# Optimization experiments

Measured on AMD Instinct MI355X. Metric: run time of the kernel, lower is better.

The kernel has to match this reference:

```python
import jax, jax.numpy as jnp
import numpy as np


def setup_inputs() -> dict:
    key = jax.random.key(0)
    k = jax.random.split(key, 5)
    B, L, D = 8, 2048, 256  # D = 2*d_model, c_len == q_len == L (required by source's s1 broadcast)
    c = jax.random.normal(k[0], (B, L, D), dtype=jnp.float32)
    q = jax.random.normal(k[1], (B, L, D), dtype=jnp.float32)
    c_weight = jax.random.normal(k[2], (D, 1), dtype=jnp.float32) * 0.05
    q_weight = jax.random.normal(k[3], (D, 1), dtype=jnp.float32) * 0.05
    cq_weight = jax.random.normal(k[4], (1, 1, D), dtype=jnp.float32) * 0.05
    bias = jnp.zeros((1,), dtype=jnp.float32)
    return {"c": c, "q": q, "c_weight": c_weight, "q_weight": q_weight,
            "cq_weight": cq_weight, "bias": bias}


def reference(c, q, c_weight, q_weight, cq_weight, bias):
    # Dropout omitted (identity) for a deterministic reference.
    # s0: [B, c_len, 1] -> broadcasts over q_len
    s0 = jnp.matmul(c, c_weight)                       # [B, L, 1]
    # s1 (faithful to source, which uses c here): [B, 1, c_len]
    s1 = jnp.swapaxes(jnp.matmul(c, q_weight), 1, 2)   # [B, 1, L]
    # s2: elementwise-scaled batched GEMM: [B, c_len, q_len]
    s2 = jnp.matmul(c * cq_weight, jnp.swapaxes(q, 1, 2))
    s = s0 + s1 + s2 + bias                            # broadcast sum + scalar bias
    return s
```

## Files before the change

### kernel.cpp

```cpp
#include <hip/hip_runtime.h>
#include <hip/hip_bf16.h>

#define B_ 8
#define L_ 2048
#define D_ 256

typedef __bf16 bf16x8 __attribute__((ext_vector_type(8)));
typedef float f32x4 __attribute__((ext_vector_type(4)));

static __device__ __forceinline__ unsigned short f2bf(float f) {
    unsigned int u = __builtin_bit_cast(unsigned int, f);
    unsigned int lsb = (u >> 16) & 1u;
    u += 0x7fffu + lsb;
    return (unsigned short)(u >> 16);
}

static __device__ __forceinline__ void gload_lds16(const void* g, void* l) {
    __builtin_amdgcn_global_load_lds(
        (const __attribute__((address_space(1))) unsigned int*)g,
        (__attribute__((address_space(3))) unsigned int*)l, 16, 0, 0);
}

__global__ __launch_bounds__(256) void prep_kernel(
    const float* __restrict__ c, const float* __restrict__ q,
    const float* __restrict__ cw, const float* __restrict__ qw,
    const float* __restrict__ cqw, const float* __restrict__ bias,
    unsigned short* __restrict__ Abf, unsigned short* __restrict__ Qbf,
    float* __restrict__ s0, float* __restrict__ s1)
{
    const int wave = threadIdx.x >> 6;
    const int lane = threadIdx.x & 63;
    const int row  = blockIdx.x * 4 + wave;

    const float4 cv  = *(const float4*)(c   + (size_t)row * D_ + lane * 4);
    const float4 qv  = *(const float4*)(q   + (size_t)row * D_ + lane * 4);
    const float4 wc  = *(const float4*)(cw  + lane * 4);
    const float4 wq  = *(const float4*)(qw  + lane * 4);
    const float4 wcq = *(const float4*)(cqw + lane * 4);

    ushort4 av, qb;
    av.x = f2bf(cv.x * wcq.x); av.y = f2bf(cv.y * wcq.y);
    av.z = f2bf(cv.z * wcq.z); av.w = f2bf(cv.w * wcq.w);
    qb.x = f2bf(qv.x); qb.y = f2bf(qv.y);
    qb.z = f2bf(qv.z); qb.w = f2bf(qv.w);
    *(ushort4*)(Abf + (size_t)row * D_ + lane * 4) = av;
    *(ushort4*)(Qbf + (size_t)row * D_ + lane * 4) = qb;

    float p0 = cv.x * wc.x + cv.y * wc.y + cv.z * wc.z + cv.w * wc.w;
    float p1 = cv.x * wq.x + cv.y * wq.y + cv.z * wq.z + cv.w * wq.w;
    #pragma unroll
    for (int off = 32; off > 0; off >>= 1) {
        p0 += __shfl_down(p0, off);
        p1 += __shfl_down(p1, off);
    }
    if (lane == 0) { s0[row] = p0 + bias[0]; s1[row] = p1; }
}

#define BM 128
#define BN 128
#define BK 32
#define NSTEP (D_ / BK)

__global__ __launch_bounds__(256, 4) void gemm_kernel(
    const unsigned short* __restrict__ A, const unsigned short* __restrict__ Q,
    const float* __restrict__ s0, const float* __restrict__ s1,
    float* __restrict__ out)
{
    __shared__ __align__(16) unsigned short As[2][BM * BK];
    __shared__ __align__(16) unsigned short Qs[2][BM * BK];

    const int tid  = threadIdx.x;
    const int wave = tid >> 6;
    const int lane = tid & 63;

    const int lin = blockIdx.x + (blockIdx.y << 4) + (blockIdx.z << 8);
    const int nl  = ((lin & 7) << 8) | (lin >> 3);
    const int b   = nl >> 8;
    const int brow = ((nl >> 4) & 15) * BM;
    const int bcol = (nl & 15) * BN;

    const unsigned short* Ab = A + ((size_t)b * L_ + brow) * D_;
    const unsigned short* Qb = Q + ((size_t)b * L_ + bcol) * D_;

    const int wr = wave >> 1;
    const int wc = wave & 1;

    const f32x4 zero = {0.f, 0.f, 0.f, 0.f};
    f32x4 acc[4][4];
    #pragma unroll
    for (int m = 0; m < 4; ++m)
        #pragma unroll
        for (int n = 0; n < 4; ++n) acc[m][n] = zero;

    auto stage = [&](int s) {
        const int k0 = s * BK;
        unsigned short* ab = &As[s & 1][0];
        unsigned short* qb = &Qs[s & 1][0];
        #pragma unroll
        for (int i = 0; i < 2; ++i) {
            const int sidx = i * 256 + wave * 64 + lane;
            const int row  = sidx >> 2;
            const int sl   = sidx & 3;
            const int ksrc = k0 + ((sl ^ ((row >> 1) & 3)) << 3);
            const int wbase = (i * 256 + wave * 64) * 8;
            gload_lds16(Ab + (size_t)row * D_ + ksrc, ab + wbase);
            gload_lds16(Qb + (size_t)row * D_ + ksrc, qb + wbase);
        }
    };

    auto compute = [&](int t) {
        const unsigned short* ab = &As[t & 1][0];
        const unsigned short* qb = &Qs[t & 1][0];
        bf16x8 af[4], qf[4];
        #pragma unroll
        for (int m = 0; m < 4; ++m) {
            const int row = wr * 64 + m * 16 + (lane & 15);
            const int idx = row * 32 + (((lane >> 4) ^ ((row >> 1) & 3)) << 3);
            af[m] = *(const bf16x8*)(ab + idx);
        }
        #pragma unroll
        for (int n = 0; n < 4; ++n) {
            const int row = wc * 64 + n * 16 + (lane & 15);
            const int idx = row * 32 + (((lane >> 4) ^ ((row >> 1) & 3)) << 3);
            qf[n] = *(const bf16x8*)(qb + idx);
        }
        __builtin_amdgcn_s_setprio(1);
        #pragma unroll
        for (int m = 0; m < 4; ++m)
            #pragma unroll
            for (int n = 0; n < 4; ++n)
                acc[m][n] = __builtin_amdgcn_mfma_f32_16x16x32_bf16(
                    af[m], qf[n], acc[m][n], 0, 0, 0);
        __builtin_amdgcn_s_setprio(0);
    };

    stage(0);

    const int cohort = lin >> 8;
    if (cohort >= 1 && cohort <= 3) {
        const unsigned long long dl = (unsigned long long)cohort * 160ULL;
        const unsigned long long t0 = __builtin_amdgcn_s_memrealtime();
        while (__builtin_amdgcn_s_memrealtime() - t0 < dl)
            __builtin_amdgcn_s_sleep(2);
    }

#define STEP(T, VM) do {                                        \
        if ((T) + 1 < NSTEP) stage((T) + 1);                    \
        asm volatile("s_waitcnt vmcnt(" #VM ")" ::: "memory");  \
        __builtin_amdgcn_s_barrier();                           \
        asm volatile("" ::: "memory");                          \
        compute(T);                                             \
        asm volatile("" ::: "memory");                          \
        __builtin_amdgcn_s_barrier();                           \
        asm volatile("" ::: "memory");                          \
    } while (0)

    STEP(0, 4); STEP(1, 4); STEP(2, 4); STEP(3, 4);
    STEP(4, 4); STEP(5, 4); STEP(6, 4); STEP(7, 0);
#undef STEP

    const float* s0b = s0 + b * L_ + brow;
    const float* s1b = s1 + b * L_ + bcol;
    float s1v[4];
    #pragma unroll
    for (int n = 0; n < 4; ++n) s1v[n] = s1b[wc * 64 + n * 16 + (lane & 15)];
    float* outb = out + ((size_t)b * L_ + brow) * L_ + bcol;
    #pragma unroll
    for (int m = 0; m < 4; ++m) {
        #pragma unroll
        for (int r = 0; r < 4; ++r) {
            const int i = wr * 64 + m * 16 + (lane >> 4) * 4 + r;
            const float s0v = s0b[i];
            float* orow = outb + (size_t)i * L_;
            #pragma unroll
            for (int n = 0; n < 4; ++n)
                orow[wc * 64 + n * 16 + (lane & 15)] = acc[m][n][r] + s0v + s1v[n];
        }
    }
}

__global__ void naive_kernel(const float* __restrict__ c, const float* __restrict__ q,
                             const float* __restrict__ cw, const float* __restrict__ qw,
                             const float* __restrict__ cqw, const float* __restrict__ bias,
                             float* __restrict__ out)
{
    const size_t total = (size_t)B_ * L_ * L_;
    for (size_t idx = (size_t)blockIdx.x * blockDim.x + threadIdx.x; idx < total;
         idx += (size_t)gridDim.x * blockDim.x) {
        const int b = (int)(idx / ((size_t)L_ * L_));
        const int rem = (int)(idx % ((size_t)L_ * L_));
        const int i = rem / L_, j = rem % L_;
        const float* ci = c + ((size_t)b * L_ + i) * D_;
        const float* cj = c + ((size_t)b * L_ + j) * D_;
        const float* qj = q + ((size_t)b * L_ + j) * D_;
        float acc = bias[0];
        for (int d = 0; d < D_; ++d)
            acc += ci[d] * cw[d] + cj[d] * qw[d] + ci[d] * cqw[d] * qj[d];
        out[idx] = acc;
    }
}

extern "C" void kernel_launch(void* const* d_in, const int* in_sizes, int n_in,
                              void* d_out, int out_size, void* d_ws, size_t ws_size,
                              hipStream_t stream) {
    const float* c    = (const float*)d_in[0];
    const float* q    = (const float*)d_in[1];
    const float* cw   = (const float*)d_in[2];
    const float* qw   = (const float*)d_in[3];
    const float* cqw  = (const float*)d_in[4];
    const float* bias = (const float*)d_in[5];
    float* out = (float*)d_out;

    const size_t bytesA = (size_t)B_ * L_ * D_ * 2;
    const size_t need   = 2 * bytesA + 2 * (size_t)B_ * L_ * 4;

    if (ws_size >= need) {
        unsigned short* Abf = (unsigned short*)d_ws;
        unsigned short* Qbf = (unsigned short*)((char*)d_ws + bytesA);
        float* s0 = (float*)((char*)d_ws + 2 * bytesA);
        float* s1 = s0 + (size_t)B_ * L_;
        prep_kernel<<<B_ * L_ / 4, 256, 0, stream>>>(c, q, cw, qw, cqw, bias,
                                                     Abf, Qbf, s0, s1);
        dim3 grid(L_ / BN, L_ / BM, B_);
        gemm_kernel<<<grid, 256, 0, stream>>>(Abf, Qbf, s0, s1, out);
    } else {
        naive_kernel<<<2048, 256, 0, stream>>>(c, q, cw, qw, cqw, bias, out);
    }
}
```

Before: 44.55 us.

## Switch GEMM to barrier-free single-wave 64x64 tiles over a flat grid

Replaces the 4-wave 128x128 block tile with one 64-thread wave per block that owns a 64x64 output tile. Each wave stages its own A/Q slices into double-buffered LDS, so the block-level barriers can be dropped and only the vmcnt wait remains. The staggered cohort sleep delay is removed, and the grid becomes a flat 8192-block launch with a batch-interleaved index mapping. In exchange, tile reuse halves, so more operand traffic goes to L2. Many more small blocks must also be scheduled, in a kernel dominated by output stores.

```diff
diff --git a/kernel.cpp b/kernel.cpp
--- a/kernel.cpp
+++ b/kernel.cpp
@@ -56,12 +56,12 @@
     if (lane == 0) { s0[row] = p0 + bias[0]; s1[row] = p1; }
 }
 
-#define BM 128
-#define BN 128
+#define BM 64
+#define BN 64
 #define BK 32
 #define NSTEP (D_ / BK)
 
-__global__ __launch_bounds__(256, 4) void gemm_kernel(
+__global__ __launch_bounds__(64, 3) void gemm_kernel(
     const unsigned short* __restrict__ A, const unsigned short* __restrict__ Q,
     const float* __restrict__ s0, const float* __restrict__ s1,
     float* __restrict__ out)
@@ -69,42 +69,35 @@
     __shared__ __align__(16) unsigned short As[2][BM * BK];
     __shared__ __align__(16) unsigned short Qs[2][BM * BK];
 
-    const int tid  = threadIdx.x;
-    const int wave = tid >> 6;
-    const int lane = tid & 63;
-
-    const int lin = blockIdx.x + (blockIdx.y << 4) + (blockIdx.z << 8);
-    const int nl  = ((lin & 7) << 8) | (lin >> 3);
-    const int b   = nl >> 8;
-    const int brow = ((nl >> 4) & 15) * BM;
-    const int bcol = (nl & 15) * BN;
+    const int lane = threadIdx.x & 63;
+
+    const int lin = blockIdx.x;
+    const int nl  = ((lin & 7) << 10) | (lin >> 3);
+    const int b    = nl >> 10;
+    const int brow = ((nl >> 5) & 31) * BM;
+    const int bcol = (nl & 31) * BN;
 
     const unsigned short* Ab = A + ((size_t)b * L_ + brow) * D_;
     const unsigned short* Qb = Q + ((size_t)b * L_ + bcol) * D_;
 
-    const int wr = wave >> 1;
-    const int wc = wave & 1;
-
-    const f32x4 zero = {0.f, 0.f, 0.f, 0.f};
     f32x4 acc[4][4];
     #pragma unroll
     for (int m = 0; m < 4; ++m)
         #pragma unroll
-        for (int n = 0; n < 4; ++n) acc[m][n] = zero;
+        for (int n = 0; n < 4; ++n) acc[m][n] = {0.f, 0.f, 0.f, 0.f};
 
     auto stage = [&](int s) {
         const int k0 = s * BK;
         unsigned short* ab = &As[s & 1][0];
         unsigned short* qb = &Qs[s & 1][0];
         #pragma unroll
-        for (int i = 0; i < 2; ++i) {
-            const int sidx = i * 256 + wave * 64 + lane;
+        for (int i = 0; i < 4; ++i) {
+            const int sidx = i * 64 + lane;
             const int row  = sidx >> 2;
             const int sl   = sidx & 3;
             const int ksrc = k0 + ((sl ^ ((row >> 1) & 3)) << 3);
-            const int wbase = (i * 256 + wave * 64) * 8;
-            gload_lds16(Ab + (size_t)row * D_ + ksrc, ab + wbase);
-            gload_lds16(Qb + (size_t)row * D_ + ksrc, qb + wbase);
+            gload_lds16(Ab + (size_t)row * D_ + ksrc, ab + i * 512);
+            gload_lds16(Qb + (size_t)row * D_ + ksrc, qb + i * 512);
         }
     };
 
@@ -114,13 +107,13 @@
         bf16x8 af[4], qf[4];
         #pragma unroll
         for (int m = 0; m < 4; ++m) {
-            const int row = wr * 64 + m * 16 + (lane & 15);
+            const int row = m * 16 + (lane & 15);
             const int idx = row * 32 + (((lane >> 4) ^ ((row >> 1) & 3)) << 3);
             af[m] = *(const bf16x8*)(ab + idx);
         }
         #pragma unroll
         for (int n = 0; n < 4; ++n) {
-            const int row = wc * 64 + n * 16 + (lane & 15);
+            const int row = n * 16 + (lane & 15);
             const int idx = row * 32 + (((lane >> 4) ^ ((row >> 1) & 3)) << 3);
             qf[n] = *(const bf16x8*)(qb + idx);
         }
@@ -136,45 +129,32 @@
 
     stage(0);
 
-    const int cohort = lin >> 8;
-    if (cohort >= 1 && cohort <= 3) {
-        const unsigned long long dl = (unsigned long long)cohort * 160ULL;
-        const unsigned long long t0 = __builtin_amdgcn_s_memrealtime();
-        while (__builtin_amdgcn_s_memrealtime() - t0 < dl)
-            __builtin_amdgcn_s_sleep(2);
-    }
-
 #define STEP(T, VM) do {                                        \
         if ((T) + 1 < NSTEP) stage((T) + 1);                    \
         asm volatile("s_waitcnt vmcnt(" #VM ")" ::: "memory");  \
-        __builtin_amdgcn_s_barrier();                           \
-        asm volatile("" ::: "memory");                          \
         compute(T);                                             \
-        asm volatile("" ::: "memory");                          \
-        __builtin_amdgcn_s_barrier();                           \
-        asm volatile("" ::: "memory");                          \
     } while (0)
 
-    STEP(0, 4); STEP(1, 4); STEP(2, 4); STEP(3, 4);
-    STEP(4, 4); STEP(5, 4); STEP(6, 4); STEP(7, 0);
+    STEP(0, 8); STEP(1, 8); STEP(2, 8); STEP(3, 8);
+    STEP(4, 8); STEP(5, 8); STEP(6, 8); STEP(7, 0);
 #undef STEP
 
     const float* s0b = s0 + b * L_ + brow;
     const float* s1b = s1 + b * L_ + bcol;
     float s1v[4];
     #pragma unroll
-    for (int n = 0; n < 4; ++n) s1v[n] = s1b[wc * 64 + n * 16 + (lane & 15)];
+    for (int n = 0; n < 4; ++n) s1v[n] = s1b[n * 16 + (lane & 15)];
     float* outb = out + ((size_t)b * L_ + brow) * L_ + bcol;
     #pragma unroll
     for (int m = 0; m < 4; ++m) {
         #pragma unroll
         for (int r = 0; r < 4; ++r) {
-            const int i = wr * 64 + m * 16 + (lane >> 4) * 4 + r;
+            const int i = m * 16 + (lane >> 4) * 4 + r;
             const float s0v = s0b[i];
             float* orow = outb + (size_t)i * L_;
             #pragma unroll
             for (int n = 0; n < 4; ++n)
-                orow[wc * 64 + n * 16 + (lane & 15)] = acc[m][n][r] + s0v + s1v[n];
+                orow[n * 16 + (lane & 15)] = acc[m][n][r] + s0v + s1v[n];
         }
     }
 }
@@ -221,8 +201,7 @@
         float* s1 = s0 + (size_t)B_ * L_;
         prep_kernel<<<B_ * L_ / 4, 256, 0, stream>>>(c, q, cw, qw, cqw, bias,
                                                      Abf, Qbf, s0, s1);
-        dim3 grid(L_ / BN, L_ / BM, B_);
-        gemm_kernel<<<grid, 256, 0, stream>>>(Abf, Qbf, s0, s1, out);
+        gemm_kernel<<<dim3(8192), 64, 0, stream>>>(Abf, Qbf, s0, s1, out);
     } else {
         naive_kernel<<<2048, 256, 0, stream>>>(c, q, cw, qw, cqw, bias, out);
     }
```

Measured after the change: 53.09 us. 1.19x slower.

## Fuse q bf16 conversion into GEMM by staging fp32 q tiles in LDS

Applied to the files above, without the earlier changes.

The prep kernel no longer converts q to bf16 and writes it to a workspace. The GEMM now loads fp32 q tiles straight into LDS using a new XOR swizzle, then converts them to bf16 in registers before the MFMA. This removes one prep-side read and write of q. In exchange, each GEMM block reads twice as many bytes for q, uses more LDS and issues more loads per stage, and converts q redundantly across the 16 row-blocks. The occupancy hint in the launch bounds is also dropped.

```diff
diff --git a/kernel.cpp b/kernel.cpp
--- a/kernel.cpp
+++ b/kernel.cpp
@@ -22,10 +22,10 @@
 }
 
 __global__ __launch_bounds__(256) void prep_kernel(
-    const float* __restrict__ c, const float* __restrict__ q,
+    const float* __restrict__ c,
     const float* __restrict__ cw, const float* __restrict__ qw,
     const float* __restrict__ cqw, const float* __restrict__ bias,
-    unsigned short* __restrict__ Abf, unsigned short* __restrict__ Qbf,
+    unsigned short* __restrict__ Abf,
     float* __restrict__ s0, float* __restrict__ s1)
 {
     const int wave = threadIdx.x >> 6;
@@ -33,18 +33,14 @@
     const int row  = blockIdx.x * 4 + wave;
 
     const float4 cv  = *(const float4*)(c   + (size_t)row * D_ + lane * 4);
-    const float4 qv  = *(const float4*)(q   + (size_t)row * D_ + lane * 4);
     const float4 wc  = *(const float4*)(cw  + lane * 4);
     const float4 wq  = *(const float4*)(qw  + lane * 4);
     const float4 wcq = *(const float4*)(cqw + lane * 4);
 
-    ushort4 av, qb;
+    ushort4 av;
     av.x = f2bf(cv.x * wcq.x); av.y = f2bf(cv.y * wcq.y);
     av.z = f2bf(cv.z * wcq.z); av.w = f2bf(cv.w * wcq.w);
-    qb.x = f2bf(qv.x); qb.y = f2bf(qv.y);
-    qb.z = f2bf(qv.z); qb.w = f2bf(qv.w);
     *(ushort4*)(Abf + (size_t)row * D_ + lane * 4) = av;
-    *(ushort4*)(Qbf + (size_t)row * D_ + lane * 4) = qb;
 
     float p0 = cv.x * wc.x + cv.y * wc.y + cv.z * wc.z + cv.w * wc.w;
     float p1 = cv.x * wq.x + cv.y * wq.y + cv.z * wq.z + cv.w * wq.w;
@@ -61,13 +57,13 @@
 #define BK 32
 #define NSTEP (D_ / BK)
 
-__global__ __launch_bounds__(256, 4) void gemm_kernel(
-    const unsigned short* __restrict__ A, const unsigned short* __restrict__ Q,
+__global__ __launch_bounds__(256) void gemm_kernel(
+    const unsigned short* __restrict__ A, const float* __restrict__ q,
     const float* __restrict__ s0, const float* __restrict__ s1,
     float* __restrict__ out)
 {
     __shared__ __align__(16) unsigned short As[2][BM * BK];
-    __shared__ __align__(16) unsigned short Qs[2][BM * BK];
+    __shared__ __align__(16) float          Qs[2][BM * BK];
 
     const int tid  = threadIdx.x;
     const int wave = tid >> 6;
@@ -80,37 +76,42 @@
     const int bcol = (nl & 15) * BN;
 
     const unsigned short* Ab = A + ((size_t)b * L_ + brow) * D_;
-    const unsigned short* Qb = Q + ((size_t)b * L_ + bcol) * D_;
+    const float*          Qb = q + ((size_t)b * L_ + bcol) * D_;
 
     const int wr = wave >> 1;
     const int wc = wave & 1;
 
-    const f32x4 zero = {0.f, 0.f, 0.f, 0.f};
     f32x4 acc[4][4];
     #pragma unroll
     for (int m = 0; m < 4; ++m)
         #pragma unroll
-        for (int n = 0; n < 4; ++n) acc[m][n] = zero;
+        for (int n = 0; n < 4; ++n) acc[m][n] = {0.f, 0.f, 0.f, 0.f};
 
     auto stage = [&](int s) {
         const int k0 = s * BK;
         unsigned short* ab = &As[s & 1][0];
-        unsigned short* qb = &Qs[s & 1][0];
+        float*          qs = &Qs[s & 1][0];
         #pragma unroll
         for (int i = 0; i < 2; ++i) {
-            const int sidx = i * 256 + wave * 64 + lane;
+            const int sidx = i * 256 + tid;
             const int row  = sidx >> 2;
             const int sl   = sidx & 3;
             const int ksrc = k0 + ((sl ^ ((row >> 1) & 3)) << 3);
-            const int wbase = (i * 256 + wave * 64) * 8;
-            gload_lds16(Ab + (size_t)row * D_ + ksrc, ab + wbase);
-            gload_lds16(Qb + (size_t)row * D_ + ksrc, qb + wbase);
+            gload_lds16(Ab + (size_t)row * D_ + ksrc, ab + (i * 256 + wave * 64) * 8);
+        }
+        #pragma unroll
+        for (int i = 0; i < 4; ++i) {
+            const int sidx = i * 256 + tid;
+            const int row  = sidx >> 3;
+            const int sl   = sidx & 7;
+            const int ksrc = k0 + ((sl ^ (row & 7)) << 2);
+            gload_lds16(Qb + (size_t)row * D_ + ksrc, qs + (i * 256 + wave * 64) * 4);
         }
     };
 
     auto compute = [&](int t) {
         const unsigned short* ab = &As[t & 1][0];
-        const unsigned short* qb = &Qs[t & 1][0];
+        const float*          qs = &Qs[t & 1][0];
         bf16x8 af[4], qf[4];
         #pragma unroll
         for (int m = 0; m < 4; ++m) {
@@ -121,8 +122,15 @@
         #pragma unroll
         for (int n = 0; n < 4; ++n) {
             const int row = wc * 64 + n * 16 + (lane & 15);
-            const int idx = row * 32 + (((lane >> 4) ^ ((row >> 1) & 3)) << 3);
-            qf[n] = *(const bf16x8*)(qb + idx);
+            const int sb  = (lane >> 4) * 2;
+            const f32x4 lo = *(const f32x4*)(qs + row * 32 + (((sb    ) ^ (row & 7)) << 2));
+            const f32x4 hi = *(const f32x4*)(qs + row * 32 + (((sb + 1) ^ (row & 7)) << 2));
+            bf16x8 v;
+            v[0] = (__bf16)lo[0]; v[1] = (__bf16)lo[1];
+            v[2] = (__bf16)lo[2]; v[3] = (__bf16)lo[3];
+            v[4] = (__bf16)hi[0]; v[5] = (__bf16)hi[1];
+            v[6] = (__bf16)hi[2]; v[7] = (__bf16)hi[3];
+            qf[n] = v;
         }
         __builtin_amdgcn_s_setprio(1);
         #pragma unroll
@@ -155,8 +163,8 @@
         asm volatile("" ::: "memory");                          \
     } while (0)
 
-    STEP(0, 4); STEP(1, 4); STEP(2, 4); STEP(3, 4);
-    STEP(4, 4); STEP(5, 4); STEP(6, 4); STEP(7, 0);
+    STEP(0, 6); STEP(1, 6); STEP(2, 6); STEP(3, 6);
+    STEP(4, 6); STEP(5, 6); STEP(6, 6); STEP(7, 0);
 #undef STEP
 
     const float* s0b = s0 + b * L_ + brow;
@@ -212,17 +220,16 @@
     float* out = (float*)d_out;
 
     const size_t bytesA = (size_t)B_ * L_ * D_ * 2;
-    const size_t need   = 2 * bytesA + 2 * (size_t)B_ * L_ * 4;
+    const size_t need   = bytesA + 2 * (size_t)B_ * L_ * 4;
 
     if (ws_size >= need) {
         unsigned short* Abf = (unsigned short*)d_ws;
-        unsigned short* Qbf = (unsigned short*)((char*)d_ws + bytesA);
-        float* s0 = (float*)((char*)d_ws + 2 * bytesA);
+        float* s0 = (float*)((char*)d_ws + bytesA);
         float* s1 = s0 + (size_t)B_ * L_;
-        prep_kernel<<<B_ * L_ / 4, 256, 0, stream>>>(c, q, cw, qw, cqw, bias,
-                                                     Abf, Qbf, s0, s1);
+        prep_kernel<<<B_ * L_ / 4, 256, 0, stream>>>(c, cw, qw, cqw, bias,
+                                                     Abf, s0, s1);
         dim3 grid(L_ / BN, L_ / BM, B_);
-        gemm_kernel<<<grid, 256, 0, stream>>>(Abf, Qbf, s0, s1, out);
+        gemm_kernel<<<grid, 256, 0, stream>>>(Abf, q, s0, s1, out);
     } else {
         naive_kernel<<<2048, 256, 0, stream>>>(c, q, cw, qw, cqw, bias, out);
     }
```

Result: slower. 49.82 us (+11.8%).
